# Kernel tuning notes

Hardware: AMD Instinct MI355X
Metric: run time of the kernel (lower is better)

The kernel has to match this reference:

```python
import jax, jax.numpy as jnp
import numpy as np

B, N, FD, HD, G = 32, 512, 768, 384, 3
ALPHA = 0.2  # LeakyReLU slope
NEG = -9e15


def layer_norm(x, g, b, eps=1e-5):
    m = jnp.mean(x, axis=-1, keepdims=True)
    v = jnp.var(x, axis=-1, keepdims=True)
    return (x - m) / jnp.sqrt(v + eps) * g + b


def gat_layer(x, adj, W, a):
    # x: [B,N,FD], adj: [N,N], W: [FD,HD], a: [2*HD]
    h = jnp.einsum('bnf,fd->bnd', x, W)  # [B,N,HD]
    # concat score decomposes: e_ij = lrelu(h_i . a[:HD] + h_j . a[HD:])
    e1 = h @ a[:HD]   # [B,N]
    e2 = h @ a[HD:]   # [B,N]
    e = jax.nn.leaky_relu(e1[:, :, None] + e2[:, None, :], ALPHA)  # [B,N,N]
    e = jnp.where(adj[None] > 0, e, NEG)
    att = jax.nn.softmax(e, axis=2)  # masked softmax over neighbors
    h_prime = jnp.einsum('bij,bjd->bid', att, h)
    return jax.nn.elu(h_prime)  # concat=True -> ELU


def setup_inputs() -> dict:
    key = jax.random.key(0)
    ks = jax.random.split(key, 10)
    s = 0.05
    return {
        'x': jax.random.normal(ks[0], (B, N, FD), jnp.float32),
        'adj': jax.random.randint(ks[1], (G, N, N), 0, 2),
        'W': jax.random.normal(ks[2], (G, FD, HD), jnp.float32) * s,
        'a': jax.random.normal(ks[3], (G, 2 * HD), jnp.float32) * s,
        'log_unc': jnp.zeros((G,), jnp.float32),
        'gate_w': jax.random.normal(ks[4], (FD, G), jnp.float32) * s,
        'gate_b': jnp.zeros((G,), jnp.float32),
        'ln1_g': jnp.ones((HD,), jnp.float32),
        'ln1_b': jnp.zeros((HD,), jnp.float32),
        'w1': jax.random.normal(ks[5], (HD, HD), jnp.float32) * s,
        'b1': jnp.zeros((HD,), jnp.float32),
        'w2': jax.random.normal(ks[6], (HD, FD), jnp.float32) * s,
        'b2': jnp.zeros((FD,), jnp.float32),
        'ln2_g': jnp.ones((FD,), jnp.float32),
        'ln2_b': jnp.zeros((FD,), jnp.float32),
    }


def reference(x, adj, W, a, log_unc, gate_w, gate_b, ln1_g, ln1_b,
              w1, b1, w2, b2, ln2_g, ln2_b):
    # global (uncertainty) weights
    unc = jnp.exp(log_unc)
    attw = jax.nn.softmax(1.0 / (unc + 1e-8))  # [G]
    # content gates from batch-averaged features
    avg = jnp.mean(x, axis=0)                          # [N,FD]
    cg = jax.nn.softmax(avg @ gate_w + gate_b, axis=-1)  # [N,G]
    # per-graph GAT + LayerNorm, vmapped over the G graphs
    gouts = jax.vmap(lambda ad, Wi, ai: layer_norm(gat_layer(x, ad, Wi, ai), ln1_g, ln1_b))(adj, W, a)  # [G,B,N,HD]
    weights = 0.7 * attw[:, None, None, None] + 0.3 * cg.T[:, None, :, None]  # [G,1|B,N,1]
    fused = jnp.sum(weights * gouts, axis=0)  # [B,N,HD]
    # output projection + LayerNorm
    proj = jax.nn.relu(fused @ w1 + b1) @ w2 + b2
    proj = layer_norm(proj, ln2_g, ln2_b)
    # residual gate
    gv = jax.nn.sigmoid(jnp.sum(proj * x, axis=-1, keepdims=True) / np.sqrt(FD).astype(np.float32))
    return gv * x + (1.0 - gv) * proj
```

## Files before the change

kernel.cpp:

```cpp
#include <hip/hip_runtime.h>

typedef unsigned short ushort_t;
typedef unsigned int uint_t;
typedef __bf16 bf16x8 __attribute__((ext_vector_type(8)));
typedef float f32x4 __attribute__((ext_vector_type(4)));
typedef unsigned int u32x4 __attribute__((ext_vector_type(4)));
typedef unsigned short u16x4 __attribute__((ext_vector_type(4)));
typedef unsigned short u16x8 __attribute__((ext_vector_type(8)));

#define B_SZ 32
#define N_SZ 512
#define FD_SZ 768
#define HD_SZ 384
#define G_SZ 3
#define M_SZ (B_SZ * N_SZ)
#define ALPHA_LR 0.2f
#define NEGV -9.0e15f
#define VTILE (HD_SZ * 32)
#define PSLICE ((size_t)M_SZ * HD_SZ)

__device__ __forceinline__ float bf2f(ushort_t u) { return __uint_as_float(((uint_t)u) << 16); }
__device__ __forceinline__ ushort_t f2bf(float f) {
  uint_t x = __float_as_uint(f);
  return (ushort_t)((x + 0x7fffu + ((x >> 16) & 1u)) >> 16);
}

__device__ __forceinline__ void gload_lds16(const ushort_t* g, ushort_t* l) {
  __builtin_amdgcn_global_load_lds(
      (const __attribute__((address_space(1))) uint_t*)(const void*)g,
      (__attribute__((address_space(3))) uint_t*)(void*)l, 16, 0, 0);
}

__global__ __launch_bounds__(256) void transpose_tile(
    const float* __restrict__ src, ushort_t* __restrict__ dst, int R, int C) {
  __shared__ float t[64][65];
  size_t base = (size_t)blockIdx.z * R * C;
  int c0 = blockIdx.x * 64, r0 = blockIdx.y * 64;
  int tx = threadIdx.x & 63, ty = threadIdx.x >> 6;
#pragma unroll
  for (int i = 0; i < 16; i++) {
    int r = ty * 16 + i;
    t[r][tx] = src[base + (size_t)(r0 + r) * C + c0 + tx];
  }
  __syncthreads();
#pragma unroll
  for (int i = 0; i < 16; i++) {
    int c = ty * 16 + i;
    dst[base + (size_t)(c0 + c) * R + r0 + tx] = f2bf(t[tx][c]);
  }
}

__global__ __launch_bounds__(256) void pack_adj(
    const int* __restrict__ adj, uint_t* __restrict__ am) {
  size_t i = (size_t)blockIdx.x * 256 + threadIdx.x;
  unsigned long long mask = __ballot(adj[i] != 0);
  int lane = threadIdx.x & 63;
  if ((lane & 31) == 0) am[i >> 5] = (uint_t)(mask >> (lane & 32));
}

__global__ __launch_bounds__(256) void zero_kernel(float* __restrict__ p) {
  p[(size_t)blockIdx.x * 256 + threadIdx.x] = 0.f;
}

__global__ __launch_bounds__(256) void gate_kernel(
    const float* __restrict__ x, const float* __restrict__ gate_w,
    const float* __restrict__ gate_b, float* __restrict__ cg,
    ushort_t* __restrict__ xb) {
  int n = blockIdx.x;
  int tid = threadIdx.x;
  float a0 = 0.f, a1 = 0.f, a2 = 0.f;
  for (int f = tid; f < FD_SZ; f += 256) {
    float s = 0.f;
#pragma unroll
    for (int b = 0; b < B_SZ; b++) {
      size_t off = ((size_t)b * N_SZ + n) * FD_SZ + f;
      float xv = x[off];
      xb[off] = f2bf(xv);
      s += xv;
    }
    float avg = s * (1.0f / B_SZ);
    a0 += avg * gate_w[f * 3 + 0];
    a1 += avg * gate_w[f * 3 + 1];
    a2 += avg * gate_w[f * 3 + 2];
  }
  for (int m = 1; m < 64; m <<= 1) {
    a0 += __shfl_xor(a0, m, 64);
    a1 += __shfl_xor(a1, m, 64);
    a2 += __shfl_xor(a2, m, 64);
  }
  __shared__ float red[3][4];
  int wave = tid >> 6, lane = tid & 63;
  if (lane == 0) { red[0][wave] = a0; red[1][wave] = a1; red[2][wave] = a2; }
  __syncthreads();
  if (tid == 0) {
    float l0 = red[0][0] + red[0][1] + red[0][2] + red[0][3] + gate_b[0];
    float l1 = red[1][0] + red[1][1] + red[1][2] + red[1][3] + gate_b[1];
    float l2 = red[2][0] + red[2][1] + red[2][2] + red[2][3] + gate_b[2];
    float mx = fmaxf(l0, fmaxf(l1, l2));
    float e0 = __expf(l0 - mx), e1 = __expf(l1 - mx), e2 = __expf(l2 - mx);
    float inv = 1.0f / (e0 + e1 + e2);
    cg[n * 3 + 0] = e0 * inv;
    cg[n * 3 + 1] = e1 * inv;
    cg[n * 3 + 2] = e2 * inv;
  }
}

template <bool RELU, bool OUTBF16, bool HASBIAS, bool VFOUT, bool EOUT, bool ARED3>
__global__ __launch_bounds__(256) void gemm_kernel(
    const ushort_t* __restrict__ Ab, size_t strideA,
    const ushort_t* __restrict__ Bt, size_t strideB,
    const float* __restrict__ bias,
    void* __restrict__ Cv, size_t strideC,
    int M, int K, int Nc,
    const float* __restrict__ av, float* __restrict__ e1,
    float* __restrict__ e2) {
  __shared__ __attribute__((aligned(16))) ushort_t As[128 * 32];
  __shared__ __attribute__((aligned(16))) ushort_t Bs[128 * 32];
  int tid = threadIdx.x, wave = tid >> 6, lane = tid & 63;
  int m0 = blockIdx.y * 128, n0 = blockIdx.x * 128;
  const ushort_t* A = Ab + (size_t)blockIdx.z * strideA;
  const ushort_t* Bb = Bt + (size_t)blockIdx.z * strideB;

  f32x4 acc[4][4];
  f32x4 z4 = {0.f, 0.f, 0.f, 0.f};
#pragma unroll
  for (int i = 0; i < 4; i++)
#pragma unroll
    for (int j = 0; j < 4; j++) acc[i][j] = z4;

  int wm = (wave & 1) * 64, wn = (wave >> 1) * 64;
  int srow = lane >> 2, schk = (lane & 3) * 8;

  for (int kt = 0; kt < K; kt += 32) {
    u32x4 aw[2];
    if (ARED3) {
#pragma unroll
      for (int i = 0; i < 2; i++) {
        const ushort_t* ap =
            A + (size_t)(m0 + wave * 32 + i * 16 + srow) * K + kt + schk;
        u16x8 q0 = *(const u16x8*)ap;
        u16x8 q1 = *(const u16x8*)(ap + PSLICE);
        u16x8 q2 = *(const u16x8*)(ap + 2 * PSLICE);
        union { ushort_t us[8]; u32x4 v; } pk;
#pragma unroll
        for (int k = 0; k < 8; k++)
          pk.us[k] = f2bf(bf2f(q0[k]) + bf2f(q1[k]) + bf2f(q2[k]));
        aw[i] = pk.v;
      }
    }
    __syncthreads();
#pragma unroll
    for (int i = 0; i < 2; i++) {
      int rowBase = wave * 32 + i * 16;
      if (ARED3) {
        *(u32x4*)(As + rowBase * 32 + lane * 8) = aw[i];
      } else {
        gload_lds16(A + (size_t)(m0 + rowBase + srow) * K + kt + schk,
                    As + rowBase * 32);
      }
      gload_lds16(Bb + (size_t)(n0 + rowBase + srow) * K + kt + schk,
                  Bs + rowBase * 32);
    }
    __syncthreads();
    bf16x8 af[4], bfr[4];
#pragma unroll
    for (int t = 0; t < 4; t++) {
      af[t] = *(const bf16x8*)(As + (wm + t * 16 + (lane & 15)) * 32 + (lane >> 4) * 8);
      bfr[t] = *(const bf16x8*)(Bs + (wn + t * 16 + (lane & 15)) * 32 + (lane >> 4) * 8);
    }
#pragma unroll
    for (int mt = 0; mt < 4; mt++)
#pragma unroll
      for (int nt = 0; nt < 4; nt++)
        acc[mt][nt] = __builtin_amdgcn_mfma_f32_16x16x32_bf16(af[mt], bfr[nt], acc[mt][nt], 0, 0, 0);
  }

  if (VFOUT) {
#pragma unroll
    for (int mt = 0; mt < 4; mt++) {
#pragma unroll
      for (int nt = 0; nt < 4; nt++) {
        int d = n0 + wn + nt * 16 + (lane & 15);
        int gm = m0 + wm + mt * 16 + (lane >> 4) * 4;
        int b = gm >> 9, jt = (gm >> 5) & 15, j2 = gm & 31;
        u16x4 pk;
#pragma unroll
        for (int r2 = 0; r2 < 4; r2++) pk[r2] = f2bf(acc[mt][nt][r2]);
        size_t off = ((size_t)((blockIdx.z * B_SZ + b) * 16 + jt)) * VTILE + (size_t)d * 32 + j2;
        *(u16x4*)((ushort_t*)Cv + off) = pk;
      }
    }
    if (EOUT) {
      int g = blockIdx.z;
      float a1v[4], a2v[4];
#pragma unroll
      for (int nt = 0; nt < 4; nt++) {
        int d = n0 + wn + nt * 16 + (lane & 15);
        a1v[nt] = av[g * 2 * HD_SZ + d];
        a2v[nt] = av[g * 2 * HD_SZ + HD_SZ + d];
      }
#pragma unroll
      for (int mt = 0; mt < 4; mt++)
#pragma unroll
        for (int r2 = 0; r2 < 4; r2++) {
          float p1 = 0.f, p2 = 0.f;
#pragma unroll
          for (int nt = 0; nt < 4; nt++) {
            p1 += acc[mt][nt][r2] * a1v[nt];
            p2 += acc[mt][nt][r2] * a2v[nt];
          }
#pragma unroll
          for (int msk = 1; msk < 16; msk <<= 1) {
            p1 += __shfl_xor(p1, msk, 64);
            p2 += __shfl_xor(p2, msk, 64);
          }
          if ((lane & 15) == 0) {
            int gm = m0 + wm + mt * 16 + (lane >> 4) * 4 + r2;
            atomicAdd(&e1[(size_t)g * M_SZ + gm], p1);
            atomicAdd(&e2[(size_t)g * M_SZ + gm], p2);
          }
        }
    }
  } else {
#pragma unroll
    for (int mt = 0; mt < 4; mt++) {
#pragma unroll
      for (int nt = 0; nt < 4; nt++) {
        int gn = n0 + wn + nt * 16 + (lane & 15);
        float bvs = HASBIAS ? bias[gn] : 0.f;
#pragma unroll
        for (int r2 = 0; r2 < 4; r2++) {
          int gm = m0 + wm + mt * 16 + (lane >> 4) * 4 + r2;
          float v = acc[mt][nt][r2] + bvs;
          if (RELU) v = v > 0.f ? v : 0.f;
          size_t off = (size_t)blockIdx.z * strideC + (size_t)gm * Nc + gn;
          if (OUTBF16) ((ushort_t*)Cv)[off] = f2bf(v);
          else ((float*)Cv)[off] = v;
        }
      }
    }
  }
}

__global__ __launch_bounds__(512, 4) void attn_kernel(
    const uint_t* __restrict__ adjm, const ushort_t* __restrict__ vf,
    const float* __restrict__ e1, const float* __restrict__ e2,
    const float* __restrict__ cg, const float* __restrict__ log_unc,
    const float* __restrict__ ln1g, const float* __restrict__ ln1b,
    ushort_t* __restrict__ pf) {
  __shared__ __attribute__((aligned(16))) ushort_t Pb[32][520];
  __shared__ float e2s[512];
  __shared__ float e1r[32];
  __shared__ uint_t amS[32][16];
  __shared__ float lng[HD_SZ], lnb[HD_SZ];
  __shared__ float cgr[32];
  __shared__ float s1s[32][8], s2s[32][8];

  int tid = threadIdx.x, wave = tid >> 6, lane = tid & 63;
  int quad = lane >> 4, l15 = lane & 15;
  int g = blockIdx.z;
  int L = blockIdx.x + (blockIdx.y << 4);
  int b = (L & 7) + ((L >> 7) << 3);
  int i0 = ((L >> 3) & 15) * 32;

  float iv0 = 1.f / (__expf(log_unc[0]) + 1e-8f);
  float iv1 = 1.f / (__expf(log_unc[1]) + 1e-8f);
  float iv2 = 1.f / (__expf(log_unc[2]) + 1e-8f);
  float mxa = fmaxf(iv0, fmaxf(iv1, iv2));
  float w0 = __expf(iv0 - mxa), w1 = __expf(iv1 - mxa), w2 = __expf(iv2 - mxa);
  float wsum = 1.f / (w0 + w1 + w2);
  float attwg = (g == 0 ? w0 : (g == 1 ? w1 : w2)) * wsum;

  if (tid < HD_SZ) {
    lng[tid] = ln1g[tid];
    lnb[tid] = ln1b[tid];
  }
  if (tid < 32) {
    cgr[tid] = cg[(i0 + tid) * 3 + g];
    e1r[tid] = e1[((size_t)g * B_SZ + b) * N_SZ + i0 + tid];
  }
  amS[tid >> 4][tid & 15] = adjm[((size_t)g * N_SZ + i0 + (tid >> 4)) * 16 + (tid & 15)];
  e2s[tid] = e2[((size_t)g * B_SZ + b) * N_SZ + tid];
  __syncthreads();

#pragma unroll
  for (int rr = 0; rr < 4; rr++) {
    int rw = wave * 4 + rr;
    float e1v = e1r[rw];
    float sv[8];
    float m = -3.0e38f;
#pragma unroll
    for (int jj = 0; jj < 8; jj++) {
      int j = lane + jj * 64;
      float s = e1v + e2s[j];
      s = s > 0.f ? s : ALPHA_LR * s;
      uint_t mw = amS[rw][(lane >> 5) + jj * 2];
      s = ((mw >> (j & 31)) & 1u) ? s : NEGV;
      sv[jj] = s;
      m = fmaxf(m, s);
    }
    for (int msk = 1; msk < 64; msk <<= 1) m = fmaxf(m, __shfl_xor(m, msk, 64));
    float sum = 0.f;
#pragma unroll
    for (int jj = 0; jj < 8; jj++) {
      float e = __expf(sv[jj] - m);
      sv[jj] = e;
      sum += e;
    }
    for (int msk = 1; msk < 64; msk <<= 1) sum += __shfl_xor(sum, msk, 64);
    float inv = 1.0f / sum;
#pragma unroll
    for (int jj = 0; jj < 8; jj++) Pb[rw][lane + jj * 64] = f2bf(sv[jj] * inv);
  }
  __syncthreads();

  f32x4 acc[2][3];
  f32x4 z4 = {0.f, 0.f, 0.f, 0.f};
#pragma unroll
  for (int mt = 0; mt < 2; mt++)
#pragma unroll
    for (int t = 0; t < 3; t++) acc[mt][t] = z4;
  const ushort_t* vbase = vf + ((size_t)(g * B_SZ + b) * 16) * VTILE;
#pragma unroll 2
  for (int j0 = 0; j0 < N_SZ; j0 += 32) {
    const ushort_t* vtile = vbase + (size_t)(j0 >> 5) * VTILE;
    bf16x8 af0 = *(const bf16x8*)(&Pb[l15][j0 + quad * 8]);
    bf16x8 af1 = *(const bf16x8*)(&Pb[16 + l15][j0 + quad * 8]);
#pragma unroll
    for (int t = 0; t < 3; t++) {
      bf16x8 bf = *(const bf16x8*)(vtile + (wave * 48 + t * 16 + l15) * 32 + quad * 8);
      acc[0][t] = __builtin_amdgcn_mfma_f32_16x16x32_bf16(af0, bf, acc[0][t], 0, 0, 0);
      acc[1][t] = __builtin_amdgcn_mfma_f32_16x16x32_bf16(af1, bf, acc[1][t], 0, 0, 0);
    }
  }

  float ps1[2][4], ps2[2][4];
#pragma unroll
  for (int mt = 0; mt < 2; mt++)
#pragma unroll
    for (int r = 0; r < 4; r++) { ps1[mt][r] = 0.f; ps2[mt][r] = 0.f; }
#pragma unroll
  for (int mt = 0; mt < 2; mt++)
#pragma unroll
    for (int t = 0; t < 3; t++)
#pragma unroll
      for (int r = 0; r < 4; r++) {
        float v = acc[mt][t][r];
        v = v > 0.f ? v : __expf(v) - 1.f;
        acc[mt][t][r] = v;
        ps1[mt][r] += v;
        ps2[mt][r] += v * v;
      }
#pragma unroll
  for (int msk = 1; msk < 16; msk <<= 1) {
#pragma unroll
    for (int mt = 0; mt < 2; mt++)
#pragma unroll
      for (int r = 0; r < 4; r++) {
        ps1[mt][r] += __shfl_xor(ps1[mt][r], msk, 64);
        ps2[mt][r] += __shfl_xor(ps2[mt][r], msk, 64);
      }
  }
  if (l15 == 0) {
#pragma unroll
    for (int mt = 0; mt < 2; mt++)
#pragma unroll
      for (int r = 0; r < 4; r++) {
        s1s[mt * 16 + quad * 4 + r][wave] = ps1[mt][r];
        s2s[mt * 16 + quad * 4 + r][wave] = ps2[mt][r];
      }
  }
  __syncthreads();
#pragma unroll
  for (int mt = 0; mt < 2; mt++)
#pragma unroll
    for (int r = 0; r < 4; r++) {
      int row = mt * 16 + quad * 4 + r;
      float S1 = 0.f, S2 = 0.f;
#pragma unroll
      for (int w = 0; w < 8; w++) {
        S1 += s1s[row][w];
        S2 += s2s[row][w];
      }
      float mean = S1 * (1.f / HD_SZ);
      float var = S2 * (1.f / HD_SZ) - mean * mean;
      float rs = rsqrtf(var + 1e-5f);
      float wgt = 0.7f * attwg + 0.3f * cgr[row];
      size_t rowo = (size_t)g * PSLICE + ((size_t)b * N_SZ + i0 + row) * HD_SZ;
#pragma unroll
      for (int t = 0; t < 3; t++) {
        int d = wave * 48 + t * 16 + l15;
        pf[rowo + d] = f2bf(wgt * ((acc[mt][t][r] - mean) * rs * lng[d] + lnb[d]));
      }
    }
}

__global__ __launch_bounds__(256) void final_kernel(
    const ushort_t* __restrict__ projbf, const float* __restrict__ x,
    const float* __restrict__ ln2g, const float* __restrict__ ln2b,
    float* __restrict__ out) {
  int row = blockIdx.x;
  int tid = threadIdx.x, wave = tid >> 6, lane = tid & 63;
  const ushort_t* pr = projbf + (size_t)row * FD_SZ;
  const float* xr = x + (size_t)row * FD_SZ;
  float v[3], xv[3];
  float s1 = 0.f, s2 = 0.f;
#pragma unroll
  for (int k = 0; k < 3; k++) {
    int c = tid + k * 256;
    v[k] = bf2f(pr[c]);
    xv[k] = xr[c];
    s1 += v[k];
    s2 += v[k] * v[k];
  }
  for (int m = 1; m < 64; m <<= 1) {
    s1 += __shfl_xor(s1, m, 64);
    s2 += __shfl_xor(s2, m, 64);
  }
  __shared__ float rs1[4], rs2[4], rdt[4];
  if (lane == 0) { rs1[wave] = s1; rs2[wave] = s2; }
  __syncthreads();
  s1 = rs1[0] + rs1[1] + rs1[2] + rs1[3];
  s2 = rs2[0] + rs2[1] + rs2[2] + rs2[3];
  float mean = s1 * (1.f / FD_SZ);
  float var = s2 * (1.f / FD_SZ) - mean * mean;
  float rstd = rsqrtf(var + 1e-5f);
  float dot = 0.f;
  float pn[3];
#pragma unroll
  for (int k = 0; k < 3; k++) {
    int c = tid + k * 256;
    pn[k] = (v[k] - mean) * rstd * ln2g[c] + ln2b[c];
    dot += pn[k] * xv[k];
  }
  for (int m = 1; m < 64; m <<= 1) dot += __shfl_xor(dot, m, 64);
  if (lane == 0) rdt[wave] = dot;
  __syncthreads();
  dot = rdt[0] + rdt[1] + rdt[2] + rdt[3];
  float gv = 1.f / (1.f + __expf(-dot * (1.0f / 27.712812921102035f)));
#pragma unroll
  for (int k = 0; k < 3; k++) {
    int c = tid + k * 256;
    out[(size_t)row * FD_SZ + c] = gv * xv[k] + (1.f - gv) * pn[k];
  }
}

extern "C" void kernel_launch(void* const* d_in, const int* in_sizes, int n_in,
                              void* d_out, int out_size, void* d_ws, size_t ws_size,
                              hipStream_t stream) {
  (void)in_sizes; (void)n_in; (void)out_size; (void)ws_size;
  const float* x = (const float*)d_in[0];
  const int* adj = (const int*)d_in[1];
  const float* W = (const float*)d_in[2];
  const float* a = (const float*)d_in[3];
  const float* log_unc = (const float*)d_in[4];
  const float* gate_w = (const float*)d_in[5];
  const float* gate_b = (const float*)d_in[6];
  const float* ln1g = (const float*)d_in[7];
  const float* ln1b = (const float*)d_in[8];
  const float* w1 = (const float*)d_in[9];
  const float* b1 = (const float*)d_in[10];
  const float* w2 = (const float*)d_in[11];
  const float* b2 = (const float*)d_in[12];
  const float* ln2g = (const float*)d_in[13];
  const float* ln2b = (const float*)d_in[14];

  char* ws = (char*)d_ws;
  ushort_t* Wt      = (ushort_t*)(ws + 0);
  uint_t*   adjm    = (uint_t*)(ws + 0);
  ushort_t* w1t     = (ushort_t*)(ws + 1769472);
  ushort_t* w2t     = (ushort_t*)(ws + 2064384);
  float*    cg      = (float*)(ws + 2654208);
  float*    e1      = (float*)(ws + 2660352);
  float*    e2      = (float*)(ws + 2856960);
  ushort_t* vf      = (ushort_t*)(ws + 15636480);
  ushort_t* t1bf    = (ushort_t*)(ws + 15636480);
  ushort_t* projbf  = (ushort_t*)(ws + 28219392);
  ushort_t* xb      = (ushort_t*)d_out;
  ushort_t* pf      = (ushort_t*)d_out;

  transpose_tile<<<dim3(HD_SZ / 64, FD_SZ / 64, 3), 256, 0, stream>>>(W, Wt, FD_SZ, HD_SZ);
  transpose_tile<<<dim3(HD_SZ / 64, HD_SZ / 64, 1), 256, 0, stream>>>(w1, w1t, HD_SZ, HD_SZ);
  transpose_tile<<<dim3(FD_SZ / 64, HD_SZ / 64, 1), 256, 0, stream>>>(w2, w2t, HD_SZ, FD_SZ);

  gate_kernel<<<dim3(N_SZ), 256, 0, stream>>>(x, gate_w, gate_b, cg, xb);

  zero_kernel<<<dim3((2 * G_SZ * M_SZ) / 256), 256, 0, stream>>>(e1);

  gemm_kernel<false, true, false, true, true, false><<<dim3(3, 128, 3), 256, 0, stream>>>(
      xb, 0, Wt, (size_t)HD_SZ * FD_SZ, nullptr, vf, 0,
      M_SZ, FD_SZ, HD_SZ, a, e1, e2);

  pack_adj<<<dim3((G_SZ * N_SZ * N_SZ) / 256), 256, 0, stream>>>(adj, adjm);

  attn_kernel<<<dim3(N_SZ / 32, B_SZ, G_SZ), 512, 0, stream>>>(
      adjm, vf, e1, e2, cg, log_unc, ln1g, ln1b, pf);

  gemm_kernel<true, true, true, false, false, true><<<dim3(3, 128, 1), 256, 0, stream>>>(
      pf, 0, w1t, 0, b1, t1bf, 0, M_SZ, HD_SZ, HD_SZ, nullptr, nullptr, nullptr);
  gemm_kernel<false, true, true, false, false, false><<<dim3(6, 128, 1), 256, 0, stream>>>(
      t1bf, 0, w2t, 0, b2, projbf, 0, M_SZ, HD_SZ, FD_SZ, nullptr, nullptr, nullptr);

  final_kernel<<<dim3(M_SZ), 256, 0, stream>>>(projbf, x, ln2g, ln2b, (float*)d_out);
}
```

Measured before the change: 327.6 us.

## Double-buffer GEMM LDS tiles to overlap next-tile loads with MFMA

The GEMM kernel's shared-memory A/B tiles become two buffers, and the next K-slice is staged while the current one feeds the MFMAs. The loop drops from two barriers per iteration to one. The aim is to hide global-to-LDS load latency behind matrix compute. In exchange, LDS use doubles, which may reduce occupancy. The async global_load_lds into the alternate buffer relies on the single barrier for correctness, so synchronization may be fragile.

```diff
diff --git a/kernel.cpp b/kernel.cpp
--- a/kernel.cpp
+++ b/kernel.cpp
@@ -18,6 +18,7 @@
 #define NEGV -9.0e15f
 #define VTILE (HD_SZ * 32)
 #define PSLICE ((size_t)M_SZ * HD_SZ)
+#define TILEE (128 * 32)
 
 __device__ __forceinline__ float bf2f(ushort_t u) { return __uint_as_float(((uint_t)u) << 16); }
 __device__ __forceinline__ ushort_t f2bf(float f) {
@@ -114,8 +115,8 @@
     int M, int K, int Nc,
     const float* __restrict__ av, float* __restrict__ e1,
     float* __restrict__ e2) {
-  __shared__ __attribute__((aligned(16))) ushort_t As[128 * 32];
-  __shared__ __attribute__((aligned(16))) ushort_t Bs[128 * 32];
+  __shared__ __attribute__((aligned(16))) ushort_t As[2 * TILEE];
+  __shared__ __attribute__((aligned(16))) ushort_t Bs[2 * TILEE];
   int tid = threadIdx.x, wave = tid >> 6, lane = tid & 63;
   int m0 = blockIdx.y * 128, n0 = blockIdx.x * 128;
   const ushort_t* A = Ab + (size_t)blockIdx.z * strideA;
@@ -131,13 +132,15 @@
   int wm = (wave & 1) * 64, wn = (wave >> 1) * 64;
   int srow = lane >> 2, schk = (lane & 3) * 8;
 
-  for (int kt = 0; kt < K; kt += 32) {
-    u32x4 aw[2];
-    if (ARED3) {
-#pragma unroll
-      for (int i = 0; i < 2; i++) {
+  auto stage = [&](int buf, int kt) {
+    ushort_t* Ad = As + buf * TILEE;
+    ushort_t* Bd = Bs + buf * TILEE;
+#pragma unroll
+    for (int i = 0; i < 2; i++) {
+      int rowBase = wave * 32 + i * 16;
+      if (ARED3) {
         const ushort_t* ap =
-            A + (size_t)(m0 + wave * 32 + i * 16 + srow) * K + kt + schk;
+            A + (size_t)(m0 + rowBase + srow) * K + kt + schk;
         u16x8 q0 = *(const u16x8*)ap;
         u16x8 q1 = *(const u16x8*)(ap + PSLICE);
         u16x8 q2 = *(const u16x8*)(ap + 2 * PSLICE);
@@ -145,34 +148,35 @@
 #pragma unroll
         for (int k = 0; k < 8; k++)
           pk.us[k] = f2bf(bf2f(q0[k]) + bf2f(q1[k]) + bf2f(q2[k]));
-        aw[i] = pk.v;
-      }
-    }
-    __syncthreads();
-#pragma unroll
-    for (int i = 0; i < 2; i++) {
-      int rowBase = wave * 32 + i * 16;
-      if (ARED3) {
-        *(u32x4*)(As + rowBase * 32 + lane * 8) = aw[i];
+        *(u32x4*)(Ad + rowBase * 32 + lane * 8) = pk.v;
       } else {
         gload_lds16(A + (size_t)(m0 + rowBase + srow) * K + kt + schk,
-                    As + rowBase * 32);
+                    Ad + rowBase * 32);
       }
       gload_lds16(Bb + (size_t)(n0 + rowBase + srow) * K + kt + schk,
-                  Bs + rowBase * 32);
-    }
+                  Bd + rowBase * 32);
+    }
+  };
+
+  stage(0, 0);
+  int cur = 0;
+  for (int kt = 0; kt < K; kt += 32) {
     __syncthreads();
+    if (kt + 32 < K) stage(cur ^ 1, kt + 32);
+    const ushort_t* Ar = As + cur * TILEE;
+    const ushort_t* Br = Bs + cur * TILEE;
     bf16x8 af[4], bfr[4];
 #pragma unroll
     for (int t = 0; t < 4; t++) {
-      af[t] = *(const bf16x8*)(As + (wm + t * 16 + (lane & 15)) * 32 + (lane >> 4) * 8);
-      bfr[t] = *(const bf16x8*)(Bs + (wn + t * 16 + (lane & 15)) * 32 + (lane >> 4) * 8);
+      af[t] = *(const bf16x8*)(Ar + (wm + t * 16 + (lane & 15)) * 32 + (lane >> 4) * 8);
+      bfr[t] = *(const bf16x8*)(Br + (wn + t * 16 + (lane & 15)) * 32 + (lane >> 4) * 8);
     }
 #pragma unroll
     for (int mt = 0; mt < 4; mt++)
 #pragma unroll
       for (int nt = 0; nt < 4; nt++)
         acc[mt][nt] = __builtin_amdgcn_mfma_f32_16x16x32_bf16(af[mt], bfr[nt], acc[mt][nt], 0, 0, 0);
+    cur ^= 1;
   }
 
   if (VFOUT) {
```

New measurement: 323.3 us. No clear change (-1.3%).
